# Kernel optimization log

Hardware: AMD Instinct MI355X
Metric: run time of the kernel (lower is better)

The kernel has to match this reference:

```python
import jax, jax.numpy as jnp
import numpy as np

FS = 512.0
N_PHA = 10
N_AMP = 10
FIR_LEN = 513  # odd, ~1 s at fs=512 -> resolves 2 Hz band edges
N_BINS = 18    # hard-coded in PAC.__init__
TEMP = 0.01    # ModulationIndex temperature (near-hard soft binning)
EPS = 1e-8


def _design_filters():
    # Windowed-sinc FIR bandpass, one kernel per band: h = lp(hi) - lp(lo), Hamming window.
    t = np.arange(FIR_LEN) - (FIR_LEN - 1) / 2.0
    win = np.hamming(FIR_LEN)
    def bp(lo, hi):
        lp = lambda fc: 2.0 * fc / FS * np.sinc(2.0 * fc / FS * t)
        return (lp(hi) - lp(lo)) * win
    pha_c = np.linspace(2.0, 20.0, N_PHA)
    amp_c = np.linspace(60.0, 160.0, N_AMP)
    bands = [(0.75 * c, 1.25 * c) for c in pha_c] + [(0.75 * c, 1.25 * c) for c in amp_c]
    return np.stack([bp(lo, hi) for lo, hi in bands]).astype(np.float32)  # (20, L)


def setup_inputs() -> dict:
    key = jax.random.key(0)
    x = jax.random.normal(key, (4, 16, 4096), dtype=jnp.float32)  # (B, C, T)
    filters = jnp.asarray(_design_filters())                      # (n_pha+n_amp, L)
    return {"x": x, "filters": filters}


def _analytic(sig):
    # FFT-based Hilbert analytic signal along last axis.
    T = sig.shape[-1]
    h = np.zeros(T, np.float32)
    h[0] = 1.0
    if T % 2 == 0:
        h[T // 2] = 1.0
        h[1:T // 2] = 2.0
    else:
        h[1:(T + 1) // 2] = 2.0
    return jnp.fft.ifft(jnp.fft.fft(sig, axis=-1) * jnp.asarray(h), axis=-1)


def reference(x, filters):
    B, C, T = x.shape
    L = filters.shape[-1]
    # Bandpass: (B*C, 1, T) x (n_bands, 1, L) -> (B*C, n_bands, T); symmetric kernels so corr == conv.
    xf = jax.lax.conv_general_dilated(
        x.reshape(-1, 1, T), filters[:, None, :],
        window_strides=(1,), padding=[(L // 2, L // 2)])
    xf = xf.reshape(B, C, -1, T)
    phase = jnp.angle(_analytic(xf[:, :, :N_PHA]))        # (B, C, P, T)
    amplitude = jnp.abs(_analytic(xf[:, :, N_PHA:]))      # (B, C, A, T)
    # Soft circular phase binning (temperature -> near one-hot).
    centers = jnp.asarray((-np.pi + 2.0 * np.pi * (np.arange(N_BINS) + 0.5) / N_BINS).astype(np.float32))
    d = jnp.mod(phase[..., None] - centers + np.pi, 2.0 * np.pi) - np.pi  # (B,C,P,T,K)
    w = jax.nn.softmax(-(d * d) / TEMP, axis=-1)
    # Mean amplitude per phase bin, per (pha, amp) band pair.
    amp_sum = jnp.einsum('bcptk,bcat->bcpak', w, amplitude)  # (B,C,P,A,K)
    cnt = w.sum(axis=-2)                                      # (B,C,P,K)
    mean_amp = amp_sum / (cnt[:, :, :, None, :] + EPS)
    p = mean_amp / (mean_amp.sum(-1, keepdims=True) + EPS)
    log_k = jnp.log(jnp.float32(N_BINS))
    mi = (log_k + (p * jnp.log(p + EPS)).sum(-1)) / log_k    # Tort MI, (B,C,P,A)
    return mi
```

## Files before the change

kernel.cpp:

```cpp
#include <hip/hip_runtime.h>
#include <math.h>

#define T_LEN 4096
#define FIR_L 513
#define N_PHA 10
#define N_AMP 10
#define N_BANDS 20
#define N_BINS 18
#define BC 64

typedef __attribute__((ext_vector_type(8))) short short8;
typedef __attribute__((ext_vector_type(4))) float f32x4;

#define ZA(i) (((i) << 1) + ((((i) >> 4)) << 1))
#define TA(m) (((m) << 1) + ((((m) >> 4)) << 1))

static __device__ __forceinline__ unsigned short f2bf(float x) {
    unsigned u = __float_as_uint(x);
    unsigned r = u + 0x7FFFu + ((u >> 16) & 1u);
    return (unsigned short)(r >> 16);
}

static __device__ __forceinline__ int digitrev12(int p) {
    unsigned rr = __brev((unsigned)p) >> 20;
    rr = ((rr & 0x555u) << 1) | ((rr & 0xAAAu) >> 1);
    return (int)rr;
}

static __device__ __forceinline__ void tw_derive(const float* tw, int m1,
        float& c1, float& s1, float& c2, float& s2, float& c3, float& s3) {
    const float2 w1 = *(const float2*)&tw[TA(m1)];
    c1 = w1.x; s1 = w1.y;
    s2 = 2.0f * s1 * c1;
    c2 = fmaf(-2.0f * s1, s1, 1.0f);
    c3 = c1 * c2 - s1 * s2;
    s3 = s1 * c2 + c1 * s2;
}

static __device__ __forceinline__ void bf_fwd(float2& A, float2& B, float2& C, float2& D,
        float c1, float s1, float c2, float s2, float c3, float s3) {
    const float t0r = A.x + C.x, t0i = A.y + C.y;
    const float t1r = A.x - C.x, t1i = A.y - C.y;
    const float t2r = B.x + D.x, t2i = B.y + D.y;
    const float t3r = B.x - D.x, t3i = B.y - D.y;
    const float y0r = t0r + t2r,  y0i = t0i + t2i;
    const float u1r = t1r + t3i, u1i = t1i - t3r;
    const float u2r = t0r - t2r, u2i = t0i - t2i;
    const float u3r = t1r - t3i, u3i = t1i + t3r;
    A = make_float2(y0r, y0i);
    B = make_float2(u1r * c1 + u1i * s1, u1i * c1 - u1r * s1);
    C = make_float2(u2r * c2 + u2i * s2, u2i * c2 - u2r * s2);
    D = make_float2(u3r * c3 + u3i * s3, u3i * c3 - u3r * s3);
}

static __device__ __forceinline__ void bf_inv(float2& A, float2& B, float2& C, float2& D,
        float c1, float s1, float c2, float s2, float c3, float s3) {
    const float tbr = B.x * c1 - B.y * s1, tbi = B.y * c1 + B.x * s1;
    const float tcr = C.x * c2 - C.y * s2, tci = C.y * c2 + C.x * s2;
    const float tdr = D.x * c3 - D.y * s3, tdi = D.y * c3 + D.x * s3;
    const float ar = A.x, ai = A.y;
    A = make_float2(ar + tbr + tcr + tdr, ai + tbi + tci + tdi);
    B = make_float2(ar - tbi - tcr + tdi, ai + tbr - tci - tdr);
    C = make_float2(ar - tbr + tcr - tdr, ai - tbi + tci - tdi);
    D = make_float2(ar + tbi - tcr - tdi, ai - tbr - tci + tdr);
}

static __device__ __forceinline__ void fft_fwd6(float* z, const float* tw, int tid) {
#pragma unroll
    for (int s = 0; s < 6; s += 2) {
        const int hl = 10 - 2 * s;
        const int h  = 1 << hl;
        const int h4 = h >> 2;
        const int kk = tid & (h4 - 1);
        const int g  = tid >> (hl - 2);
        const int i0 = (g << (hl + 2)) + kk;
        float2 e[4][4];
#pragma unroll
        for (int j = 0; j < 4; ++j)
#pragma unroll
            for (int r = 0; r < 4; ++r)
                e[j][r] = *(const float2*)&z[ZA(i0 + j * h4 + r * h)];
#pragma unroll
        for (int j = 0; j < 4; ++j) {
            float c1, s1, c2, s2, c3, s3;
            tw_derive(tw, (kk + j * h4) << (2 * s), c1, s1, c2, s2, c3, s3);
            bf_fwd(e[j][0], e[j][1], e[j][2], e[j][3], c1, s1, c2, s2, c3, s3);
        }
        {
            float c1, s1, c2, s2, c3, s3;
            tw_derive(tw, kk << (2 * s + 2), c1, s1, c2, s2, c3, s3);
#pragma unroll
            for (int r = 0; r < 4; ++r)
                bf_fwd(e[0][r], e[1][r], e[2][r], e[3][r], c1, s1, c2, s2, c3, s3);
        }
#pragma unroll
        for (int j = 0; j < 4; ++j)
#pragma unroll
            for (int r = 0; r < 4; ++r)
                *(float2*)&z[ZA(i0 + j * h4 + r * h)] = e[j][r];
        __syncthreads();
    }
}

static __device__ __forceinline__ void fft_inv6(float* z, const float* tw, int tid) {
#pragma unroll
    for (int s = 0; s < 6; s += 2) {
        const int L  = 1 << (2 * s);
        const int k  = tid & (L - 1);
        const int g  = tid >> (2 * s);
        const int i0 = (g << (2 * s + 4)) + k;
        float2 e[4][4];
#pragma unroll
        for (int j = 0; j < 4; ++j)
#pragma unroll
            for (int r = 0; r < 4; ++r)
                e[j][r] = *(const float2*)&z[ZA(i0 + j * L + (r << (2 * s + 2)))];
        {
            float c1, s1, c2, s2, c3, s3;
            tw_derive(tw, k << (10 - 2 * s), c1, s1, c2, s2, c3, s3);
#pragma unroll
            for (int r = 0; r < 4; ++r)
                bf_inv(e[0][r], e[1][r], e[2][r], e[3][r], c1, s1, c2, s2, c3, s3);
        }
#pragma unroll
        for (int j = 0; j < 4; ++j) {
            float c1, s1, c2, s2, c3, s3;
            tw_derive(tw, (k + j * L) << (8 - 2 * s), c1, s1, c2, s2, c3, s3);
            bf_inv(e[j][0], e[j][1], e[j][2], e[j][3], c1, s1, c2, s2, c3, s3);
        }
#pragma unroll
        for (int j = 0; j < 4; ++j)
#pragma unroll
            for (int r = 0; r < 4; ++r)
                *(float2*)&z[ZA(i0 + j * L + (r << (2 * s + 2)))] = e[j][r];
        __syncthreads();
    }
}

__global__ __launch_bounds__(256) void spectral_pre(
    const float* __restrict__ x,
    const float* __restrict__ filt,
    float2* __restrict__ Xs,
    float2* __restrict__ Hs)
{
    __shared__ float smem[10880];
    __shared__ float fb[FIR_L];
    float* z  = smem;
    float* tw = smem + 8704;

    const int tid = threadIdx.x;
    const int b   = blockIdx.x;

    for (int m = tid; m < 1024; m += 256) {
        float ang = (float)m * (6.283185307179586f / 4096.0f);
        float s, c;
        sincosf(ang, &s, &c);
        tw[TA(m)]     = c;
        tw[TA(m) + 1] = s;
    }

    if (b < BC) {
        const float* xrow = x + b * T_LEN;
        for (int i = tid; i < 4096; i += 256)
            *(float2*)&z[ZA(i)] = make_float2(xrow[i], 0.0f);
    } else {
        const int band = b - BC;
        for (int i = tid; i < FIR_L; i += 256) fb[i] = filt[band * FIR_L + i];
        __syncthreads();
        for (int i = tid; i < 4096; i += 256) {
            float hv = 0.0f;
            if (i < 257)        hv = fb[256 - i];
            else if (i >= 3840) hv = fb[4352 - i];
            *(float2*)&z[ZA(i)] = make_float2(hv, 0.0f);
        }
    }
    __syncthreads();

    fft_fwd6(z, tw, tid);

    float2* dst = (b < BC) ? (Xs + b * 4096) : (Hs + (b - BC) * 4096);
    for (int i = tid; i < 4096; i += 256)
        dst[i] = *(const float2*)&z[ZA(i)];
}

__global__ __launch_bounds__(256, 3) void spectral_main(
    const float* __restrict__ x,
    const float* __restrict__ filt,
    const float2* __restrict__ Xs,
    const float2* __restrict__ Hs,
    float* __restrict__ pha,
    unsigned short* __restrict__ amp_bf)
{
    __shared__ float smem[10880];
    __shared__ float xe[512];
    __shared__ float fb[FIR_L];
    float* z  = smem;
    float* tw = smem + 8704;

    const int tid  = threadIdx.x;
    const int bc   = blockIdx.x / N_BANDS;
    const int band = blockIdx.x % N_BANDS;

    for (int m = tid; m < 1024; m += 256) {
        float ang = (float)m * (6.283185307179586f / 4096.0f);
        float s, c;
        sincosf(ang, &s, &c);
        tw[TA(m)]     = c;
        tw[TA(m) + 1] = s;
    }

    const float* xrow = x + bc * T_LEN;
    for (int i = tid; i < 512; i += 256)
        xe[i] = (i < 256) ? xrow[i] : xrow[3584 + i];
    for (int i = tid; i < FIR_L; i += 256) fb[i] = filt[band * FIR_L + i];
    __syncthreads();

    float cf = 0.0f, ct = 0.0f;
    for (int l = 0; l <= 255 - tid; ++l)
        cf = fmaf(fb[l], xe[256 + tid + l], cf);
    for (int j = 0; j <= tid; ++j)
        ct = fmaf(fb[512 - tid + j], xe[j], ct);

    for (int i = tid; i < 4096; i += 256)
        *(float2*)&z[ZA(i)] = make_float2(0.0f, 0.0f);
    *(float2*)&z[ZA(tid)]        = make_float2(-cf, 0.0f);
    *(float2*)&z[ZA(3840 + tid)] = make_float2(-ct, 0.0f);
    __syncthreads();

    fft_fwd6(z, tw, tid);

    const float2* Xrow = Xs + bc * 4096;
    const float2* Hrow = Hs + band * 4096;
    for (int i = tid; i < 4096; i += 256) {
        const float2 X = Xrow[i];
        const float2 H = Hrow[i];
        const float2 C = *(const float2*)&z[ZA(i)];
        float pr = X.x * H.x - X.y * H.y + C.x;
        float pi = X.x * H.y + X.y * H.x + C.y;
        const int f = digitrev12(i);
        const float mf = (f == 0 || f == 2048) ? 1.0f : (f < 2048 ? 2.0f : 0.0f);
        *(float2*)&z[ZA(i)] = make_float2(pr * mf, pi * mf);
    }
    __syncthreads();

    fft_inv6(z, tw, tid);

    const float inv_n = 1.0f / 4096.0f;
    if (band < N_PHA) {
        float* dst = pha + (bc * N_PHA + band) * T_LEN;
        for (int i = tid; i < 4096; i += 256) {
            const float2 zz = *(const float2*)&z[ZA(i)];
            dst[i] = atan2f(zz.y, zz.x);
        }
    } else {
        unsigned short* dst = amp_bf + (bc * N_AMP + (band - N_PHA)) * T_LEN;
        for (int i = tid; i < 4096; i += 256) {
            const float2 zz = *(const float2*)&z[ZA(i)];
            dst[i] = f2bf(sqrtf(zz.x * zz.x + zz.y * zz.y) * inv_n);
        }
    }
}

__global__ __launch_bounds__(256) void bin_mi_mfma(
    const float* __restrict__ pha,
    const unsigned short* __restrict__ amp_bf,
    float* __restrict__ out)
{
    const int tid  = threadIdx.x;
    const int lane = tid & 63;
    const int wv   = tid >> 6;
    const int bc   = blockIdx.x / N_PHA;
    const int p    = blockIdx.x % N_PHA;

    __shared__ unsigned int wbufW[4][18 * 68];
    __shared__ float psum[4][11][N_BINS];
    __shared__ float asum[11][N_BINS];

    const float* phrow = pha + (bc * N_PHA + p) * T_LEN;
    const unsigned short* arow = amp_bf + bc * N_AMP * T_LEN;

    const float PI_F  = 3.14159274101257324f;
    const float INVD  = 2.8647889756541160f;
    const float DELTA = 0.34906585039886590f;
    const float C1    = 12.184696791468343f;
    const float C2    = 69.813170079773180f;

    const int m_ = lane & 15;
    const int q_ = lane >> 4;
    const int n_ = lane & 15;

    short8 zero8;
#pragma unroll
    for (int j = 0; j < 8; ++j) zero8[j] = 0;
    short8 ones8;
#pragma unroll
    for (int j = 0; j < 8; ++j) ones8[j] = (short)0x3F80;

    f32x4 acc0 = {0.f, 0.f, 0.f, 0.f};
    f32x4 acc1 = {0.f, 0.f, 0.f, 0.f};

    const int base_t = wv * 1024;
    unsigned short* wh = (unsigned short*)&wbufW[wv][0];

    float2 pp[8];
#pragma unroll
    for (int c = 0; c < 8; ++c)
        pp[c] = *(const float2*)&phrow[base_t + c * 128 + lane * 2];

    for (int chunk = 0; chunk < 8; ++chunk) {
        const int cb = base_t + chunk * 128;

        short8 af[4];
#pragma unroll
        for (int s = 0; s < 4; ++s) {
            const int tA = cb + s * 32 + q_ * 8;
            if (m_ < N_AMP)       af[s] = *(const short8*)(arow + m_ * T_LEN + tA);
            else if (m_ == N_AMP) af[s] = ones8;
            else                  af[s] = zero8;
        }

#pragma unroll
        for (int k = 0; k < N_BINS; ++k)
            wbufW[wv][k * 68 + lane] = 0u;

#pragma unroll
        for (int h = 0; h < 2; ++h) {
            const float ph = h ? pp[chunk].y : pp[chunk].x;
            float u  = (ph + PI_F) * INVD;
            float jf = floorf(u);
            float d  = (u - jf - 0.5f) * DELTA;
            int j0 = (int)jf;
            if (j0 >= N_BINS) j0 -= N_BINS;
            const int jm = (j0 == 0) ? N_BINS - 1 : j0 - 1;
            const int jp = (j0 == N_BINS - 1) ? 0 : j0 + 1;
            const float em = expf(-C1 - C2 * d);
            const float ep = expf(-C1 + C2 * d);
            const float inv = 1.0f / (1.0f + em + ep);
            wh[(j0 * 68 + lane) * 2 + h] = f2bf(inv);
            wh[(jm * 68 + lane) * 2 + h] = f2bf(em * inv);
            wh[(jp * 68 + lane) * 2 + h] = f2bf(ep * inv);
        }
        __builtin_amdgcn_wave_barrier();

#pragma unroll
        for (int s = 0; s < 4; ++s) {
            const int woff = s * 16 + q_ * 4;
            short8 bfrag0 = *(const short8*)&wbufW[wv][n_ * 68 + woff];
            short8 bfrag1 = (n_ < 2)
                ? *(const short8*)&wbufW[wv][(16 + n_) * 68 + woff]
                : zero8;
            acc0 = __builtin_amdgcn_mfma_f32_16x16x32_bf16(af[s], bfrag0, acc0, 0, 0, 0);
            acc1 = __builtin_amdgcn_mfma_f32_16x16x32_bf16(af[s], bfrag1, acc1, 0, 0, 0);
        }
        __builtin_amdgcn_wave_barrier();
    }

#pragma unroll
    for (int r = 0; r < 4; ++r) {
        const int m = q_ * 4 + r;
        if (m < 11) {
            psum[wv][m][n_] = acc0[r];
            if (n_ < 2) psum[wv][m][16 + n_] = acc1[r];
        }
    }
    __syncthreads();

    if (tid < 11 * N_BINS) {
        const int m = tid / N_BINS;
        const int k = tid % N_BINS;
        asum[m][k] = psum[0][m][k] + psum[1][m][k] + psum[2][m][k] + psum[3][m][k];
    }
    __syncthreads();

    if (tid < N_AMP) {
        float ma[N_BINS];
        float msum = 0.0f;
#pragma unroll
        for (int k = 0; k < N_BINS; ++k) {
            float m = asum[tid][k] / (asum[10][k] + 1e-8f);
            ma[k] = m;
            msum += m;
        }
        const float inv = 1.0f / (msum + 1e-8f);
        float acc = 0.0f;
#pragma unroll
        for (int k = 0; k < N_BINS; ++k) {
            float pk = ma[k] * inv;
            acc = fmaf(pk, logf(pk + 1e-8f), acc);
        }
        const float logk = 2.89037175789124f;
        out[(bc * N_PHA + p) * N_AMP + tid] = (logk + acc) / logk;
    }
}

extern "C" void kernel_launch(void* const* d_in, const int* in_sizes, int n_in,
                              void* d_out, int out_size, void* d_ws, size_t ws_size,
                              hipStream_t stream) {
    const float* x    = (const float*)d_in[0];
    const float* filt = (const float*)d_in[1];
    float* out = (float*)d_out;

    float* pha = (float*)d_ws;
    unsigned short* amp_bf = (unsigned short*)(pha + BC * N_PHA * T_LEN);
    float2* Xs = (float2*)(amp_bf + BC * N_AMP * T_LEN);
    float2* Hs = Xs + BC * 4096;

    spectral_pre <<<BC + N_BANDS, 256, 0, stream>>>(x, filt, Xs, Hs);
    spectral_main<<<BC * N_BANDS, 256, 0, stream>>>(x, filt, Xs, Hs, pha, amp_bf);
    bin_mi_mfma  <<<BC * N_PHA,   256, 0, stream>>>(pha, amp_bf, out);
}
```

Baseline: 124.2 us.

## Move twiddles to global table, sparse first FFT pass, widen binning blocks

Twiddle factors are now computed once by an extra block of the pre kernel into a global table, and the main spectral kernel reads them from there instead of rebuilding them in shared memory with sincos. This shrinks its LDS use, and the launch-bounds occupancy hint rises from 3 to 4 blocks. The first radix-16 forward FFT pass for the sparse edge-correction signal is computed directly from its two nonzero values, which skips zero-filling the buffer and one barrier. The binning kernel uses 512 threads so each wave handles half as many time samples, at the cost of a larger cross-wave reduction.

```diff
diff --git a/kernel.cpp b/kernel.cpp
--- a/kernel.cpp
+++ b/kernel.cpp
@@ -13,7 +13,8 @@
 typedef __attribute__((ext_vector_type(4))) float f32x4;
 
 #define ZA(i) (((i) << 1) + ((((i) >> 4)) << 1))
-#define TA(m) (((m) << 1) + ((((m) >> 4)) << 1))
+
+__device__ float2 twg_dev[1024];
 
 static __device__ __forceinline__ unsigned short f2bf(float x) {
     unsigned u = __float_as_uint(x);
@@ -27,14 +28,18 @@
     return (int)rr;
 }
 
-static __device__ __forceinline__ void tw_derive(const float* tw, int m1,
+static __device__ __forceinline__ void tw_derive(const float2* tw, int m1,
         float& c1, float& s1, float& c2, float& s2, float& c3, float& s3) {
-    const float2 w1 = *(const float2*)&tw[TA(m1)];
+    const float2 w1 = tw[m1];
     c1 = w1.x; s1 = w1.y;
     s2 = 2.0f * s1 * c1;
     c2 = fmaf(-2.0f * s1, s1, 1.0f);
     c3 = c1 * c2 - s1 * s2;
     s3 = s1 * c2 + c1 * s2;
+}
+
+static __device__ __forceinline__ float2 cmul_em(float2 u, float c, float s) {
+    return make_float2(u.x * c + u.y * s, u.y * c - u.x * s);
 }
 
 static __device__ __forceinline__ void bf_fwd(float2& A, float2& B, float2& C, float2& D,
@@ -65,9 +70,9 @@
     D = make_float2(ar + tbi - tcr - tdi, ai - tbr - tci + tdr);
 }
 
-static __device__ __forceinline__ void fft_fwd6(float* z, const float* tw, int tid) {
-#pragma unroll
-    for (int s = 0; s < 6; s += 2) {
+static __device__ __forceinline__ void fft_fwd_passes(float* z, const float2* tw,
+                                                      int tid, int s0) {
+    for (int s = s0; s < 6; s += 2) {
         const int hl = 10 - 2 * s;
         const int h  = 1 << hl;
         const int h4 = h >> 2;
@@ -102,7 +107,40 @@
     }
 }
 
-static __device__ __forceinline__ void fft_inv6(float* z, const float* tw, int tid) {
+static __device__ __forceinline__ void fft_fwd_pass1_sparse(
+        float* z, const float2* tw, int tid, float2 F, float2 Tl) {
+    float c1, s1, c2, s2, c3, s3;
+    tw_derive(tw, tid, c1, s1, c2, s2, c3, s3);
+    float2 P[4];
+    P[0] = F;
+    P[1] = cmul_em(F, c1, s1);
+    P[2] = cmul_em(F, c2, s2);
+    P[3] = cmul_em(F, c3, s3);
+    tw_derive(tw, tid + 768, c1, s1, c2, s2, c3, s3);
+    const float2 iT  = make_float2(-Tl.y,  Tl.x);
+    const float2 nT  = make_float2(-Tl.x, -Tl.y);
+    const float2 niT = make_float2( Tl.y, -Tl.x);
+    float2 Q[4];
+    Q[0] = Tl;
+    Q[1] = cmul_em(iT,  c1, s1);
+    Q[2] = cmul_em(nT,  c2, s2);
+    Q[3] = cmul_em(niT, c3, s3);
+    tw_derive(tw, tid << 2, c1, s1, c2, s2, c3, s3);
+#pragma unroll
+    for (int r = 0; r < 4; ++r) {
+        const int ib = tid + (r << 10);
+        const float2 A = make_float2(P[r].x + Q[r].x, P[r].y + Q[r].y);
+        const float2 B = cmul_em(make_float2(P[r].x - Q[r].y, P[r].y + Q[r].x), c1, s1);
+        const float2 C = cmul_em(make_float2(P[r].x - Q[r].x, P[r].y - Q[r].y), c2, s2);
+        const float2 D = cmul_em(make_float2(P[r].x + Q[r].y, P[r].y - Q[r].x), c3, s3);
+        *(float2*)&z[ZA(ib)]        = A;
+        *(float2*)&z[ZA(ib + 256)]  = B;
+        *(float2*)&z[ZA(ib + 512)]  = C;
+        *(float2*)&z[ZA(ib + 768)]  = D;
+    }
+}
+
+static __device__ __forceinline__ void fft_inv6(float* z, const float2* tw, int tid) {
 #pragma unroll
     for (int s = 0; s < 6; s += 2) {
         const int L  = 1 << (2 * s);
@@ -143,20 +181,28 @@
     float2* __restrict__ Xs,
     float2* __restrict__ Hs)
 {
-    __shared__ float smem[10880];
+    __shared__ float z[8704];
+    __shared__ float2 twl[1024];
     __shared__ float fb[FIR_L];
-    float* z  = smem;
-    float* tw = smem + 8704;
 
     const int tid = threadIdx.x;
     const int b   = blockIdx.x;
+
+    if (b == BC + N_BANDS) {
+        for (int m = tid; m < 1024; m += 256) {
+            float ang = (float)m * (6.283185307179586f / 4096.0f);
+            float s, c;
+            sincosf(ang, &s, &c);
+            twg_dev[m] = make_float2(c, s);
+        }
+        return;
+    }
 
     for (int m = tid; m < 1024; m += 256) {
         float ang = (float)m * (6.283185307179586f / 4096.0f);
         float s, c;
         sincosf(ang, &s, &c);
-        tw[TA(m)]     = c;
-        tw[TA(m) + 1] = s;
+        twl[m] = make_float2(c, s);
     }
 
     if (b < BC) {
@@ -176,14 +222,14 @@
     }
     __syncthreads();
 
-    fft_fwd6(z, tw, tid);
+    fft_fwd_passes(z, twl, tid, 0);
 
     float2* dst = (b < BC) ? (Xs + b * 4096) : (Hs + (b - BC) * 4096);
     for (int i = tid; i < 4096; i += 256)
         dst[i] = *(const float2*)&z[ZA(i)];
 }
 
-__global__ __launch_bounds__(256, 3) void spectral_main(
+__global__ __launch_bounds__(256, 4) void spectral_main(
     const float* __restrict__ x,
     const float* __restrict__ filt,
     const float2* __restrict__ Xs,
@@ -191,23 +237,14 @@
     float* __restrict__ pha,
     unsigned short* __restrict__ amp_bf)
 {
-    __shared__ float smem[10880];
+    __shared__ float z[8704];
     __shared__ float xe[512];
     __shared__ float fb[FIR_L];
-    float* z  = smem;
-    float* tw = smem + 8704;
 
     const int tid  = threadIdx.x;
     const int bc   = blockIdx.x / N_BANDS;
     const int band = blockIdx.x % N_BANDS;
-
-    for (int m = tid; m < 1024; m += 256) {
-        float ang = (float)m * (6.283185307179586f / 4096.0f);
-        float s, c;
-        sincosf(ang, &s, &c);
-        tw[TA(m)]     = c;
-        tw[TA(m) + 1] = s;
-    }
+    const float2* tw = twg_dev;
 
     const float* xrow = x + bc * T_LEN;
     for (int i = tid; i < 512; i += 256)
@@ -221,13 +258,9 @@
     for (int j = 0; j <= tid; ++j)
         ct = fmaf(fb[512 - tid + j], xe[j], ct);
 
-    for (int i = tid; i < 4096; i += 256)
-        *(float2*)&z[ZA(i)] = make_float2(0.0f, 0.0f);
-    *(float2*)&z[ZA(tid)]        = make_float2(-cf, 0.0f);
-    *(float2*)&z[ZA(3840 + tid)] = make_float2(-ct, 0.0f);
-    __syncthreads();
-
-    fft_fwd6(z, tw, tid);
+    fft_fwd_pass1_sparse(z, tw, tid, make_float2(-cf, 0.0f), make_float2(-ct, 0.0f));
+    __syncthreads();
+    fft_fwd_passes(z, tw, tid, 2);
 
     const float2* Xrow = Xs + bc * 4096;
     const float2* Hrow = Hs + band * 4096;
@@ -261,7 +294,7 @@
     }
 }
 
-__global__ __launch_bounds__(256) void bin_mi_mfma(
+__global__ __launch_bounds__(512) void bin_mi_mfma(
     const float* __restrict__ pha,
     const unsigned short* __restrict__ amp_bf,
     float* __restrict__ out)
@@ -272,8 +305,8 @@
     const int bc   = blockIdx.x / N_PHA;
     const int p    = blockIdx.x % N_PHA;
 
-    __shared__ unsigned int wbufW[4][18 * 68];
-    __shared__ float psum[4][11][N_BINS];
+    __shared__ unsigned int wbufW[8][18 * 68];
+    __shared__ float psum[8][11][N_BINS];
     __shared__ float asum[11][N_BINS];
 
     const float* phrow = pha + (bc * N_PHA + p) * T_LEN;
@@ -299,15 +332,15 @@
     f32x4 acc0 = {0.f, 0.f, 0.f, 0.f};
     f32x4 acc1 = {0.f, 0.f, 0.f, 0.f};
 
-    const int base_t = wv * 1024;
+    const int base_t = wv * 512;
     unsigned short* wh = (unsigned short*)&wbufW[wv][0];
 
-    float2 pp[8];
-#pragma unroll
-    for (int c = 0; c < 8; ++c)
+    float2 pp[4];
+#pragma unroll
+    for (int c = 0; c < 4; ++c)
         pp[c] = *(const float2*)&phrow[base_t + c * 128 + lane * 2];
 
-    for (int chunk = 0; chunk < 8; ++chunk) {
+    for (int chunk = 0; chunk < 4; ++chunk) {
         const int cb = base_t + chunk * 128;
 
         short8 af[4];
@@ -368,7 +401,10 @@
     if (tid < 11 * N_BINS) {
         const int m = tid / N_BINS;
         const int k = tid % N_BINS;
-        asum[m][k] = psum[0][m][k] + psum[1][m][k] + psum[2][m][k] + psum[3][m][k];
+        float s = 0.0f;
+#pragma unroll
+        for (int w = 0; w < 8; ++w) s += psum[w][m][k];
+        asum[m][k] = s;
     }
     __syncthreads();
 
@@ -405,7 +441,7 @@
     float2* Xs = (float2*)(amp_bf + BC * N_AMP * T_LEN);
     float2* Hs = Xs + BC * 4096;
 
-    spectral_pre <<<BC + N_BANDS, 256, 0, stream>>>(x, filt, Xs, Hs);
+    spectral_pre <<<BC + N_BANDS + 1, 256, 0, stream>>>(x, filt, Xs, Hs);
     spectral_main<<<BC * N_BANDS, 256, 0, stream>>>(x, filt, Xs, Hs, pha, amp_bf);
-    bin_mi_mfma  <<<BC * N_PHA,   256, 0, stream>>>(pha, amp_bf, out);
-}
+    bin_mi_mfma  <<<BC * N_PHA,   512, 0, stream>>>(pha, amp_bf, out);
+}
```

After: 118.2 us. 4.8% less time.
